# Performance work log

Measured on AMD Instinct MI355X. Metric: run time of the kernel, lower is better.

## Reference

```python
import jax, jax.numpy as jnp
import numpy as np
import math

def setup_inputs() -> dict:
    key = jax.random.key(0)
    k1, k2, k3, k4 = jax.random.split(key, 4)
    B, I, O, D, K, H, W = 8, 512, 512, 512, 3, 64, 64
    return {
        "x": jax.random.normal(k1, (B, I, H, W), dtype=jnp.float32),
        "dlatents_in": jax.random.normal(k2, (B, D), dtype=jnp.float32),
        "w": jax.random.normal(k3, (O, I, K, K), dtype=jnp.float32),
        "dense_w": jax.random.normal(k4, (I, D), dtype=jnp.float32),
        "dense_b": jnp.ones((I,), dtype=jnp.float32),  # bias_init=1
    }

def reference(x, dlatents_in, w, dense_w, dense_b):
    # Dense_layer: F.linear(dlatents, dense_w) * (1/sqrt(D)) + b (act=linear, lrmul=1)
    D = dlatents_in.shape[1]
    dense_scale = 1.0 / math.sqrt(D)
    style = dlatents_in @ dense_w.T * dense_scale + dense_b  # [B, I]

    O, I, K, _ = w.shape
    conv_scale = 1.0 / math.sqrt(I * K * K)  # self.scale

    # Demodulation factor: d_bo = rsqrt(sum_{ikk} (w * style_bi * scale)^2 + 1e-8)
    # computed without materializing the per-sample [B,O,I,K,K] weight.
    w2 = jnp.sum(w * w, axis=(2, 3))  # [O, I]
    d = jax.lax.rsqrt(jnp.einsum('oi,bi->bo', w2, style * style) * (conv_scale ** 2) + 1e-8)  # [B, O]

    # conv(x, w*style) == conv(x*style, w): scale input channels per-sample,
    # single shared-weight conv (padding = K//2 -> same spatial size), scale output by d.
    xs = x * style[:, :, None, None]
    pad = K // 2
    out = jax.lax.conv_general_dilated(
        xs, w * conv_scale,
        window_strides=(1, 1),
        padding=((pad, pad), (pad, pad)),
        dimension_numbers=('NCHW', 'OIHW', 'NCHW'))
    return out * d[:, :, None, None]
```

## Files before the change

kernel.cpp:

```cpp
#include <hip/hip_runtime.h>
#include <math.h>


typedef short short8 __attribute__((ext_vector_type(8)));
typedef float floatx4 __attribute__((ext_vector_type(4)));
typedef unsigned short ushort_t;

#define CIN   512
#define COUT  512

__device__ __forceinline__ ushort_t f2bf(float f) {
    union { float f; unsigned u; } v; v.f = f;
    unsigned r = v.u + 0x7fff + ((v.u >> 16) & 1);
    return (ushort_t)(r >> 16);
}

__device__ __forceinline__ void gload_lds16(const void* g, void* l) {
    __builtin_amdgcn_global_load_lds(
        (const __attribute__((address_space(1))) unsigned int*)g,
        (__attribute__((address_space(3))) unsigned int*)l, 16, 0, 0);
}

__global__ void style_kernel(const float* __restrict__ dl,
                             const float* __restrict__ dw,
                             const float* __restrict__ db,
                             float* __restrict__ style) {
    int gw   = (blockIdx.x * blockDim.x + threadIdx.x) >> 6;
    int lane = threadIdx.x & 63;
    int b = gw >> 9;
    int i = gw & 511;
    const float* dlp = dl + b * 512;
    const float* dwp = dw + (size_t)i * 512;
    float acc = 0.f;
    #pragma unroll
    for (int d = 0; d < 512; d += 64) acc += dlp[d + lane] * dwp[d + lane];
    #pragma unroll
    for (int off = 32; off > 0; off >>= 1) acc += __shfl_down(acc, off, 64);
    if (lane == 0) style[b * 512 + i] = acc * 0.044194173824159216f + db[i];
}

__global__ void w2_kernel(const float* __restrict__ w, float* __restrict__ w2) {
    int idx = blockIdx.x * blockDim.x + threadIdx.x;
    const float* wp = w + (size_t)idx * 9;
    float s = 0.f;
    #pragma unroll
    for (int t = 0; t < 9; t++) s += wp[t] * wp[t];
    w2[idx] = s;
}

__global__ void demod_kernel(const float* __restrict__ w2,
                             const float* __restrict__ style,
                             float* __restrict__ dvec) {
    int gw   = (blockIdx.x * blockDim.x + threadIdx.x) >> 6;
    int lane = threadIdx.x & 63;
    int b = gw >> 9;
    int o = gw & 511;
    const float* w2p = w2 + (size_t)o * 512;
    const float* stp = style + b * 512;
    float acc = 0.f;
    #pragma unroll
    for (int i = 0; i < 512; i += 64) {
        float s = stp[i + lane];
        acc += w2p[i + lane] * s * s;
    }
    #pragma unroll
    for (int off = 32; off > 0; off >>= 1) acc += __shfl_down(acc, off, 64);
    if (lane == 0)
        dvec[b * 512 + o] = rsqrtf(acc * (1.0f / 4608.0f) + 1e-8f);
}

__global__ void pack_w_kernel(const float* __restrict__ w, ushort_t* __restrict__ wpk) {
    int t = blockIdx.x * 256 + threadIdx.x;
    int L  = t & 63;
    int r  = t >> 6;
    int osub = r & 31;
    int r2 = r >> 5;
    int tap = r2 % 9;
    int ck  = r2 / 9;
    int o = osub * 16 + (L & 15);
    int ibase = ck * 32 + (L >> 4) * 8;
    const float cs = 0.014731391274719738f;
    short8 v;
    #pragma unroll
    for (int j = 0; j < 8; j++)
        v[j] = (short)f2bf(w[((size_t)o * 512 + ibase + j) * 9 + tap] * cs);
    *(short8*)(wpk + (size_t)t * 8) = v;
}

__global__ void pack_x_kernel(const float* __restrict__ x, const float* __restrict__ style,
                              ushort_t* __restrict__ xsg) {
    int t = blockIdx.x * 256 + threadIdx.x;
    int wp = t % 66;
    int t2 = t / 66;
    int hp = t2 % 66;
    int t3 = t2 / 66;
    int khi = t3 & 3;
    int t4 = t3 >> 2;
    int ck = t4 & 15;
    int b  = t4 >> 4;
    short8 v;
    if (hp >= 1 && hp <= 64 && wp >= 1 && wp <= 64) {
        #pragma unroll
        for (int j = 0; j < 8; j++) {
            int i = ck * 32 + khi * 8 + j;
            float f = x[(((size_t)b * 512 + i) * 64 + hp - 1) * 64 + wp - 1] * style[b * 512 + i];
            v[j] = (short)f2bf(f);
        }
    } else {
        #pragma unroll
        for (int j = 0; j < 8; j++) v[j] = 0;
    }
    *(short8*)(xsg + (size_t)t * 8) = v;
}

__global__ __launch_bounds__(256, 2) void conv_mfma_kernel(
        const ushort_t* __restrict__ xsg, const ushort_t* __restrict__ wpk,
        const float* __restrict__ dvec, float* __restrict__ out) {
    __shared__ ushort_t lds_x[4 * 6 * 66 * 8];

    const int tid  = threadIdx.x;
    const int lane = tid & 63;
    const int wv   = tid >> 6;
    const int quad = lane >> 4;
    const int l16  = lane & 15;
    const int hq = blockIdx.x;
    const int b  = blockIdx.y;
    const int og = blockIdx.z;
    const int h0 = hq * 4;

    const int mbase = (wv & 1) * 4;
    const int nbase = (wv >> 1) * 8;

    floatx4 acc[4][8];
    #pragma unroll
    for (int i = 0; i < 4; i++)
        #pragma unroll
        for (int j = 0; j < 8; j++) acc[i][j] = (floatx4)(0.f);

    const size_t img_base = (size_t)b * 16 * (4 * 66 * 66 * 8);
    const int bl_base = quad * 3168 + l16 * 8;

    for (int ck = 0; ck < 16; ck++) {
        __syncthreads();
        const ushort_t* src = xsg + img_base + (size_t)ck * (4 * 66 * 66 * 8)
                              + h0 * (66 * 8);
        for (int off = tid * 16; off < 25344; off += 4096) {
            int khi = off / 6336;
            int rem = off - khi * 6336;
            gload_lds16(src + (size_t)khi * (66 * 66 * 8) + (rem >> 1),
                        (char*)lds_x + off);
        }
        __syncthreads();

        const ushort_t* wck = wpk + (size_t)ck * (9 * 32 * 64 * 8)
                              + (og * 8 + mbase) * (64 * 8) + lane * 8;
        #pragma unroll
        for (int tap = 0; tap < 9; tap++) {
            const int dy = tap / 3, dx = tap % 3;
            short8 afr[4];
            #pragma unroll
            for (int mi = 0; mi < 4; mi++)
                afr[mi] = *(const short8*)(wck + (size_t)tap * (32 * 64 * 8) + mi * (64 * 8));
            #pragma unroll
            for (int q = 0; q < 8; q++) {
                const int nsub = nbase + q;
                const int off = bl_base + ((nsub >> 2) + dy) * 528 + ((nsub & 3) * 16 + dx) * 8;
                const short8 bfr = *(const short8*)&lds_x[off];
                #pragma unroll
                for (int mi = 0; mi < 4; mi++)
                    acc[mi][q] = __builtin_amdgcn_mfma_f32_16x16x32_bf16(
                        afr[mi], bfr, acc[mi][q], 0, 0, 0);
            }
        }
    }

    const float* dvb = dvec + b * COUT;
    #pragma unroll
    for (int mi = 0; mi < 4; mi++) {
        const int obase = (og * 8 + mbase + mi) * 16 + quad * 4;
        #pragma unroll
        for (int q = 0; q < 8; q++) {
            const int nsub = nbase + q;
            const int h = h0 + (nsub >> 2);
            const int col = (nsub & 3) * 16 + l16;
            #pragma unroll
            for (int r = 0; r < 4; r++) {
                const int o = obase + r;
                out[(((size_t)b * COUT + o) * 64 + h) * 64 + col] = acc[mi][q][r] * dvb[o];
            }
        }
    }
}

extern "C" void kernel_launch(void* const* d_in, const int* in_sizes, int n_in,
                              void* d_out, int out_size, void* d_ws, size_t ws_size,
                              hipStream_t stream) {
    const float* x  = (const float*)d_in[0];
    const float* dl = (const float*)d_in[1];
    const float* w  = (const float*)d_in[2];
    const float* dw = (const float*)d_in[3];
    const float* db = (const float*)d_in[4];
    float* out = (float*)d_out;

    float* style = (float*)d_ws;
    float* dvec  = style + 4096;
    float* w2    = style + 8192;
    ushort_t* wpk = (ushort_t*)((char*)d_ws + (2u << 20));
    ushort_t* xsg = (ushort_t*)((char*)d_ws + (8u << 20));

    style_kernel<<<dim3(1024), dim3(256), 0, stream>>>(dl, dw, db, style);
    w2_kernel   <<<dim3(1024), dim3(256), 0, stream>>>(w, w2);
    demod_kernel<<<dim3(1024), dim3(256), 0, stream>>>(w2, style, dvec);
    pack_w_kernel<<<dim3(1152), dim3(256), 0, stream>>>(w, wpk);
    pack_x_kernel<<<dim3(8712), dim3(256), 0, stream>>>(x, style, xsg);
    conv_mfma_kernel<<<dim3(16, 8, 4), dim3(256), 0, stream>>>(xsg, wpk, dvec, out);
}
```

Measured before the change: 260.6 us.

## Double-buffer conv LDS staging, prefetch weight fragments, merge prep kernels, vectorize x packing

The conv kernel now double-buffers the input tile in LDS, so the global-to-LDS load for the next channel chunk overlaps MFMA work on the current one. It also prefetches the next tap's weight fragments into registers. The six launches drop to four by merging style with w2 and demod with weight packing. pack_x now has each thread read float4s from x and write four padded columns. The costs are twice the LDS footprint, which may affect the two-blocks-per-CU occupancy, and higher register pressure from the prefetched fragments.

```diff
diff --git a/kernel.cpp b/kernel.cpp
--- a/kernel.cpp
+++ b/kernel.cpp
@@ -6,7 +6,6 @@
 typedef float floatx4 __attribute__((ext_vector_type(4)));
 typedef unsigned short ushort_t;
 
-#define CIN   512
 #define COUT  512
 
 __device__ __forceinline__ ushort_t f2bf(float f) {
@@ -21,102 +20,124 @@
         (__attribute__((address_space(3))) unsigned int*)l, 16, 0, 0);
 }
 
-__global__ void style_kernel(const float* __restrict__ dl,
-                             const float* __restrict__ dw,
-                             const float* __restrict__ db,
-                             float* __restrict__ style) {
-    int gw   = (blockIdx.x * blockDim.x + threadIdx.x) >> 6;
-    int lane = threadIdx.x & 63;
-    int b = gw >> 9;
-    int i = gw & 511;
-    const float* dlp = dl + b * 512;
-    const float* dwp = dw + (size_t)i * 512;
-    float acc = 0.f;
-    #pragma unroll
-    for (int d = 0; d < 512; d += 64) acc += dlp[d + lane] * dwp[d + lane];
-    #pragma unroll
-    for (int off = 32; off > 0; off >>= 1) acc += __shfl_down(acc, off, 64);
-    if (lane == 0) style[b * 512 + i] = acc * 0.044194173824159216f + db[i];
-}
-
-__global__ void w2_kernel(const float* __restrict__ w, float* __restrict__ w2) {
-    int idx = blockIdx.x * blockDim.x + threadIdx.x;
-    const float* wp = w + (size_t)idx * 9;
-    float s = 0.f;
-    #pragma unroll
-    for (int t = 0; t < 9; t++) s += wp[t] * wp[t];
-    w2[idx] = s;
-}
-
-__global__ void demod_kernel(const float* __restrict__ w2,
-                             const float* __restrict__ style,
-                             float* __restrict__ dvec) {
-    int gw   = (blockIdx.x * blockDim.x + threadIdx.x) >> 6;
-    int lane = threadIdx.x & 63;
-    int b = gw >> 9;
-    int o = gw & 511;
-    const float* w2p = w2 + (size_t)o * 512;
-    const float* stp = style + b * 512;
-    float acc = 0.f;
-    #pragma unroll
-    for (int i = 0; i < 512; i += 64) {
-        float s = stp[i + lane];
-        acc += w2p[i + lane] * s * s;
-    }
-    #pragma unroll
-    for (int off = 32; off > 0; off >>= 1) acc += __shfl_down(acc, off, 64);
-    if (lane == 0)
-        dvec[b * 512 + o] = rsqrtf(acc * (1.0f / 4608.0f) + 1e-8f);
-}
-
-__global__ void pack_w_kernel(const float* __restrict__ w, ushort_t* __restrict__ wpk) {
-    int t = blockIdx.x * 256 + threadIdx.x;
-    int L  = t & 63;
-    int r  = t >> 6;
-    int osub = r & 31;
-    int r2 = r >> 5;
-    int tap = r2 % 9;
-    int ck  = r2 / 9;
-    int o = osub * 16 + (L & 15);
-    int ibase = ck * 32 + (L >> 4) * 8;
-    const float cs = 0.014731391274719738f;
-    short8 v;
-    #pragma unroll
-    for (int j = 0; j < 8; j++)
-        v[j] = (short)f2bf(w[((size_t)o * 512 + ibase + j) * 9 + tap] * cs);
-    *(short8*)(wpk + (size_t)t * 8) = v;
+__global__ void style_w2_kernel(const float* __restrict__ dl,
+                                const float* __restrict__ dw,
+                                const float* __restrict__ db,
+                                const float* __restrict__ w,
+                                float* __restrict__ style,
+                                float* __restrict__ w2) {
+    if (blockIdx.x < 1024) {
+        int gw   = (blockIdx.x * 256 + threadIdx.x) >> 6;
+        int lane = threadIdx.x & 63;
+        int b = gw >> 9;
+        int i = gw & 511;
+        const float* dlp = dl + b * 512;
+        const float* dwp = dw + (size_t)i * 512;
+        float acc = 0.f;
+        #pragma unroll
+        for (int d = 0; d < 512; d += 64) acc += dlp[d + lane] * dwp[d + lane];
+        #pragma unroll
+        for (int off = 32; off > 0; off >>= 1) acc += __shfl_down(acc, off, 64);
+        if (lane == 0) style[b * 512 + i] = acc * 0.044194173824159216f + db[i];
+    } else {
+        int idx = (blockIdx.x - 1024) * 256 + threadIdx.x;
+        const float* wp = w + (size_t)idx * 9;
+        float s = 0.f;
+        #pragma unroll
+        for (int t = 0; t < 9; t++) s += wp[t] * wp[t];
+        w2[idx] = s;
+    }
+}
+
+__global__ void demod_packw_kernel(const float* __restrict__ w2,
+                                   const float* __restrict__ style,
+                                   const float* __restrict__ w,
+                                   float* __restrict__ dvec,
+                                   ushort_t* __restrict__ wpk) {
+    if (blockIdx.x < 1024) {
+        int gw   = (blockIdx.x * 256 + threadIdx.x) >> 6;
+        int lane = threadIdx.x & 63;
+        int b = gw >> 9;
+        int o = gw & 511;
+        const float* w2p = w2 + (size_t)o * 512;
+        const float* stp = style + b * 512;
+        float acc = 0.f;
+        #pragma unroll
+        for (int i = 0; i < 512; i += 64) {
+            float s = stp[i + lane];
+            acc += w2p[i + lane] * s * s;
+        }
+        #pragma unroll
+        for (int off = 32; off > 0; off >>= 1) acc += __shfl_down(acc, off, 64);
+        if (lane == 0)
+            dvec[b * 512 + o] = rsqrtf(acc * (1.0f / 4608.0f) + 1e-8f);
+    } else {
+        int t = (blockIdx.x - 1024) * 256 + threadIdx.x;
+        int L  = t & 63;
+        int r  = t >> 6;
+        int osub = r & 31;
+        int r2 = r >> 5;
+        int tap = r2 % 9;
+        int ck  = r2 / 9;
+        int o = osub * 16 + (L & 15);
+        int ibase = ck * 32 + (L >> 4) * 8;
+        const float cs = 0.014731391274719738f;
+        short8 v;
+        #pragma unroll
+        for (int j = 0; j < 8; j++)
+            v[j] = (short)f2bf(w[((size_t)o * 512 + ibase + j) * 9 + tap] * cs);
+        *(short8*)(wpk + (size_t)t * 8) = v;
+    }
 }
 
 __global__ void pack_x_kernel(const float* __restrict__ x, const float* __restrict__ style,
                               ushort_t* __restrict__ xsg) {
-    int t = blockIdx.x * 256 + threadIdx.x;
-    int wp = t % 66;
-    int t2 = t / 66;
+    int t  = blockIdx.x * 256 + threadIdx.x;
+    int g  = t % 17;
+    int t2 = t / 17;
     int hp = t2 % 66;
     int t3 = t2 / 66;
     int khi = t3 & 3;
     int t4 = t3 >> 2;
     int ck = t4 & 15;
     int b  = t4 >> 4;
-    short8 v;
-    if (hp >= 1 && hp <= 64 && wp >= 1 && wp <= 64) {
+    size_t rowbase = (((size_t)(b * 16 + ck) * 4 + khi) * 66 + hp) * 66 * 8;
+    if (g == 16) {
+        short8 z = (short8)0;
+        *(short8*)(xsg + rowbase) = z;
+        *(short8*)(xsg + rowbase + 65 * 8) = z;
+        return;
+    }
+    int wp0 = 1 + g * 4;
+    short8 v[4];
+    if (hp >= 1 && hp <= 64) {
         #pragma unroll
         for (int j = 0; j < 8; j++) {
             int i = ck * 32 + khi * 8 + j;
-            float f = x[(((size_t)b * 512 + i) * 64 + hp - 1) * 64 + wp - 1] * style[b * 512 + i];
-            v[j] = (short)f2bf(f);
+            const float4 xv = *(const float4*)&x[(((size_t)b * 512 + i) * 64 + hp - 1) * 64 + wp0 - 1];
+            const float s = style[b * 512 + i];
+            v[0][j] = (short)f2bf(xv.x * s);
+            v[1][j] = (short)f2bf(xv.y * s);
+            v[2][j] = (short)f2bf(xv.z * s);
+            v[3][j] = (short)f2bf(xv.w * s);
         }
     } else {
         #pragma unroll
-        for (int j = 0; j < 8; j++) v[j] = 0;
-    }
-    *(short8*)(xsg + (size_t)t * 8) = v;
-}
-
+        for (int p = 0; p < 4; p++)
+            #pragma unroll
+            for (int j = 0; j < 8; j++) v[p][j] = 0;
+    }
+    #pragma unroll
+    for (int p = 0; p < 4; p++)
+        *(short8*)(xsg + rowbase + (size_t)(wp0 + p) * 8) = v[p];
+}
+
+#define CKSTR  147456
+#define TAPSTR 16384
 __global__ __launch_bounds__(256, 2) void conv_mfma_kernel(
         const ushort_t* __restrict__ xsg, const ushort_t* __restrict__ wpk,
         const float* __restrict__ dvec, float* __restrict__ out) {
-    __shared__ ushort_t lds_x[4 * 6 * 66 * 8];
+    __shared__ ushort_t lds_x[2][4 * 6 * 66 * 8];
 
     const int tid  = threadIdx.x;
     const int lane = tid & 63;
@@ -137,41 +158,58 @@
         #pragma unroll
         for (int j = 0; j < 8; j++) acc[i][j] = (floatx4)(0.f);
 
-    const size_t img_base = (size_t)b * 16 * (4 * 66 * 66 * 8);
+    const size_t img_base = (size_t)b * 16 * (4 * 66 * 66 * 8) + h0 * (66 * 8);
     const int bl_base = quad * 3168 + l16 * 8;
+
+    auto stage = [&](int ck, ushort_t* dst) {
+        const ushort_t* src = xsg + img_base + (size_t)ck * (4 * 66 * 66 * 8);
+        #pragma unroll
+        for (int k = 0; k < 7; k++) {
+            int off = tid * 16 + k * 4096;
+            if (off < 25344) {
+                int khi = off / 6336;
+                int rem = off - khi * 6336;
+                gload_lds16(src + (size_t)khi * (66 * 66 * 8) + (rem >> 1),
+                            (char*)dst + off);
+            }
+        }
+    };
+
+    const ushort_t* wlane = wpk + (size_t)(og * 8 + mbase) * 512 + lane * 8;
+    short8 a_cur[4], a_nxt[4];
+    #pragma unroll
+    for (int mi = 0; mi < 4; mi++) a_cur[mi] = *(const short8*)(wlane + mi * 512);
+
+    stage(0, lds_x[0]);
+    int buf = 0;
 
     for (int ck = 0; ck < 16; ck++) {
         __syncthreads();
-        const ushort_t* src = xsg + img_base + (size_t)ck * (4 * 66 * 66 * 8)
-                              + h0 * (66 * 8);
-        for (int off = tid * 16; off < 25344; off += 4096) {
-            int khi = off / 6336;
-            int rem = off - khi * 6336;
-            gload_lds16(src + (size_t)khi * (66 * 66 * 8) + (rem >> 1),
-                        (char*)lds_x + off);
-        }
-        __syncthreads();
-
-        const ushort_t* wck = wpk + (size_t)ck * (9 * 32 * 64 * 8)
-                              + (og * 8 + mbase) * (64 * 8) + lane * 8;
+        if (ck < 15) stage(ck + 1, lds_x[buf ^ 1]);
+        const ushort_t* lp  = lds_x[buf];
+        const ushort_t* wck = wlane + (size_t)ck * CKSTR;
         #pragma unroll
         for (int tap = 0; tap < 9; tap++) {
             const int dy = tap / 3, dx = tap % 3;
-            short8 afr[4];
+            const ushort_t* wnx = (tap < 8) ? (wck + (tap + 1) * TAPSTR)
+                                            : (wck + (ck < 15 ? CKSTR : 0));
             #pragma unroll
             for (int mi = 0; mi < 4; mi++)
-                afr[mi] = *(const short8*)(wck + (size_t)tap * (32 * 64 * 8) + mi * (64 * 8));
+                a_nxt[mi] = *(const short8*)(wnx + mi * 512);
             #pragma unroll
             for (int q = 0; q < 8; q++) {
                 const int nsub = nbase + q;
                 const int off = bl_base + ((nsub >> 2) + dy) * 528 + ((nsub & 3) * 16 + dx) * 8;
-                const short8 bfr = *(const short8*)&lds_x[off];
+                const short8 bfr = *(const short8*)&lp[off];
                 #pragma unroll
                 for (int mi = 0; mi < 4; mi++)
                     acc[mi][q] = __builtin_amdgcn_mfma_f32_16x16x32_bf16(
-                        afr[mi], bfr, acc[mi][q], 0, 0, 0);
+                        a_cur[mi], bfr, acc[mi][q], 0, 0, 0);
             }
-        }
+            #pragma unroll
+            for (int mi = 0; mi < 4; mi++) a_cur[mi] = a_nxt[mi];
+        }
+        buf ^= 1;
     }
 
     const float* dvb = dvec + b * COUT;
@@ -208,10 +246,8 @@
     ushort_t* wpk = (ushort_t*)((char*)d_ws + (2u << 20));
     ushort_t* xsg = (ushort_t*)((char*)d_ws + (8u << 20));
 
-    style_kernel<<<dim3(1024), dim3(256), 0, stream>>>(dl, dw, db, style);
-    w2_kernel   <<<dim3(1024), dim3(256), 0, stream>>>(w, w2);
-    demod_kernel<<<dim3(1024), dim3(256), 0, stream>>>(w2, style, dvec);
-    pack_w_kernel<<<dim3(1152), dim3(256), 0, stream>>>(w, wpk);
-    pack_x_kernel<<<dim3(8712), dim3(256), 0, stream>>>(x, style, xsg);
-    conv_mfma_kernel<<<dim3(16, 8, 4), dim3(256), 0, stream>>>(xsg, wpk, dvec, out);
-}
+    style_w2_kernel  <<<dim3(2048), dim3(256), 0, stream>>>(dl, dw, db, w, style, w2);
+    demod_packw_kernel<<<dim3(2176), dim3(256), 0, stream>>>(w2, style, w, dvec, wpk);
+    pack_x_kernel    <<<dim3(2244), dim3(256), 0, stream>>>(x, style, xsg);
+    conv_mfma_kernel <<<dim3(16, 8, 4), dim3(256), 0, stream>>>(xsg, wpk, dvec, out);
+}
```

Measured after the change: 248.1 us. -4.8%, faster.
